# Kernel optimization log

Hardware: AMD Instinct MI355X
Metric: run time of the kernel (lower is better)

The kernel has to match this reference:

```python
import jax, jax.numpy as jnp
import numpy as np

N = 65536          # rays per batch
NC = 64            # coarse samples (config.num_samples_coarse)
NF = 128           # fine samples (config.num_samples_fine)
NEAR, FAR = 0.1, 1000.0


def setup_inputs() -> dict:
    key = jax.random.key(0)
    k = jax.random.split(key, 7)
    ray_origins = jax.random.normal(k[0], (N, 3), jnp.float32)
    ray_directions = jax.random.normal(k[1], (N, 3), jnp.float32)
    # stratified coarse t_vals == sample_points_along_rays(stratified=True)
    t = NEAR + (FAR - NEAR) * jnp.linspace(0.0, 1.0, NC, dtype=jnp.float32)
    t = jnp.broadcast_to(t, (N, NC))
    mids = 0.5 * (t[:, 1:] + t[:, :-1])
    upper = jnp.concatenate([mids, t[:, -1:]], axis=-1)
    lower = jnp.concatenate([t[:, :1], mids], axis=-1)
    t_rand = jax.random.uniform(k[2], (N, NC), jnp.float32)
    coarse_t_vals = lower + (upper - lower) * t_rand
    coarse_weights = jax.random.uniform(k[3], (N, NC), jnp.float32)
    u = jax.random.uniform(k[4], (N, NF), jnp.float32)
    colors = jax.random.uniform(k[5], (N, NC + NF, 3), jnp.float32)
    densities = jax.random.uniform(k[6], (N, NC + NF, 1), jnp.float32)
    return {"ray_origins": ray_origins, "ray_directions": ray_directions,
            "coarse_weights": coarse_weights, "coarse_t_vals": coarse_t_vals,
            "u": u, "colors": colors, "densities": densities}


def _hierarchical_sampling(ray_origins, ray_directions, coarse_weights, coarse_t_vals, u):
    # inverse-CDF importance resampling (GridNeRFRenderer.hierarchical_sampling)
    w = coarse_weights + 1e-5
    pdf = w / jnp.sum(w, axis=-1, keepdims=True)                 # [N, NC]
    cdf = jnp.cumsum(pdf, axis=-1)
    cdf = jnp.concatenate([jnp.zeros_like(cdf[..., :1]), cdf], axis=-1)  # [N, NC+1]
    # per-ray searchsorted (right)
    indices = jax.vmap(lambda c, uu: jnp.searchsorted(c, uu, side="right"))(cdf, u)  # [N, NF]
    nc = coarse_t_vals.shape[-1]
    below = jnp.clip(indices - 1, 0, nc - 1)
    above = jnp.clip(indices, 0, nc - 1)
    cdf_b = jnp.take_along_axis(cdf, below, axis=1)
    cdf_a = jnp.take_along_axis(cdf, above, axis=1)
    t_b = jnp.take_along_axis(coarse_t_vals, below, axis=1)
    t_a = jnp.take_along_axis(coarse_t_vals, above, axis=1)
    denom = cdf_a - cdf_b
    denom = jnp.where(denom < 1e-5, jnp.ones_like(denom), denom)
    tt = (u - cdf_b) / denom
    fine_t_vals = t_b + tt * (t_a - t_b)
    combined_t_vals = jnp.sort(jnp.concatenate([coarse_t_vals, fine_t_vals], axis=-1), axis=-1)  # [N, NC+NF]
    fine_points = ray_origins[:, None, :] + ray_directions[:, None, :] * combined_t_vals[..., None]
    return fine_points, combined_t_vals


def _volume_rendering(colors, densities, t_vals, ray_directions):
    dists = t_vals[..., 1:] - t_vals[..., :-1]
    dists = jnp.concatenate([dists, jnp.full_like(dists[..., :1], 1e10)], axis=-1)
    dists = dists * jnp.linalg.norm(ray_directions, axis=-1, keepdims=True)   # [N, S]
    alpha = 1.0 - jnp.exp(-densities[..., 0] * dists)                         # [N, S]
    # exclusive cumprod transmittance (== cumprod + roll + T[...,0]=1)
    trans = jnp.cumprod(1.0 - alpha + 1e-10, axis=-1)
    trans = jnp.concatenate([jnp.ones_like(trans[..., :1]), trans[..., :-1]], axis=-1)
    weights = alpha * trans
    rgb = jnp.sum(weights[..., None] * colors, axis=-2)   # [N, 3]
    depth = jnp.sum(weights * t_vals, axis=-1)            # [N]
    opacity = jnp.sum(weights, axis=-1)                   # [N]
    return rgb, depth, opacity, weights


def reference(ray_origins, ray_directions, coarse_weights, coarse_t_vals, u, colors, densities):
    fine_points, combined_t_vals = _hierarchical_sampling(
        ray_origins, ray_directions, coarse_weights, coarse_t_vals, u)
    rgb, depth, opacity, weights = _volume_rendering(
        colors, densities, combined_t_vals, ray_directions)
    return (rgb, depth, opacity, fine_points)
```

## Files before the change

kernel.cpp:

```cpp
#include <hip/hip_runtime.h>
#include <math.h>


#define NRAYS 65536
#define NCC   64
#define NFF   128
#define SS    192

__global__ __launch_bounds__(256)
void nerf_fused(const float* __restrict__ ro,  const float* __restrict__ rd,
                const float* __restrict__ cw,  const float* __restrict__ ct,
                const float* __restrict__ uu,  const float* __restrict__ col,
                const float* __restrict__ den, float* __restrict__ out)
{
    const int lane = threadIdx.x & 63;
    const int wv   = threadIdx.x >> 6;
    const int ray  = blockIdx.x * 4 + wv;

    __shared__ float s_cdf[4][65];
    __shared__ float s_ct [4][64];
    __shared__ float s_su [4][128];
    __shared__ float s_vals[4][256];

    float wt = cw[(size_t)ray * NCC + lane] + 1e-5f;
    float tc = ct[(size_t)ray * NCC + lane];
    float x = wt;
    #pragma unroll
    for (int off = 1; off < 64; off <<= 1) {
        float y = __shfl_up(x, off);
        if (lane >= off) x += y;
    }
    float total = __shfl(x, 63);
    float cv = x / total;
    #pragma unroll
    for (int off = 1; off < 64; off <<= 1) {
        float y = __shfl_up(cv, off);
        if (lane >= off) cv = fmaxf(cv, y);
    }
    s_cdf[wv][lane + 1] = cv;
    if (lane == 0) s_cdf[wv][0] = 0.0f;
    s_ct[wv][lane] = tc;

    float2 u2 = *(const float2*)(uu + (size_t)ray * NFF + 2 * lane);
    float v0 = u2.x, v1 = u2.y;
    #pragma unroll
    for (int k = 2; k <= 128; k <<= 1) {
        #pragma unroll
        for (int j = k >> 1; j >= 1; j >>= 1) {
            bool up = (((lane << 1) & k) == 0);
            if (j == 1) {
                float a = v0, b = v1;
                v0 = up ? fminf(a, b) : fmaxf(a, b);
                v1 = up ? fmaxf(a, b) : fminf(a, b);
            } else {
                int m = j >> 1;
                bool keepmin = (((lane & m) == 0) == up);
                float p0 = __shfl_xor(v0, m);
                float p1 = __shfl_xor(v1, m);
                v0 = keepmin ? fminf(v0, p0) : fmaxf(v0, p0);
                v1 = keepmin ? fminf(v1, p1) : fmaxf(v1, p1);
            }
        }
    }
    *(float2*)&s_su[wv][2 * lane] = make_float2(v0, v1);

    const float* cdfp = s_cdf[wv];
    const float* ctp  = s_ct[wv];
    float us[2] = {v0, v1};
    #pragma unroll
    for (int q = 0; q < 2; ++q) {
        float u = us[q];
        int pos = 0;
        #pragma unroll
        for (int st = 32; st >= 1; st >>= 1) {
            int np = pos + st;
            pos = (cdfp[np] <= u) ? np : pos;
        }
        int above = (pos + 1 < 63) ? (pos + 1) : 63;
        float cb = cdfp[pos], ca = cdfp[above];
        float tb = ctp[pos],  ta = ctp[above];
        float dnm = ca - cb;
        dnm = (dnm < 1e-5f) ? 1.0f : dnm;
        float tt = (u - cb) / dnm;
        float fval = tb + tt * (ta - tb);
        int rank = 2 * lane + q + pos + 1;
        s_vals[wv][rank] = fval;
    }

    const float* sup = s_su[wv];
    float key = cdfp[lane];
    int cnt = 0;
    #pragma unroll
    for (int st = 128; st >= 1; st >>= 1) {
        int np = cnt + st;
        bool ok = (np <= 128) && (sup[np - 1] < key);
        cnt = ok ? np : cnt;
    }
    s_vals[wv][lane + cnt] = tc;
    s_vals[wv][192 + lane] = 0.0f;

    float4 sv = *(const float4*)&s_vals[wv][4 * lane];
    float v[4] = {sv.x, sv.y, sv.z, sv.w};

    float dx = rd[(size_t)ray * 3 + 0], dy = rd[(size_t)ray * 3 + 1], dz = rd[(size_t)ray * 3 + 2];
    float ox = ro[(size_t)ray * 3 + 0], oy = ro[(size_t)ray * 3 + 1], oz = ro[(size_t)ray * 3 + 2];
    float nrm = sqrtf(dx * dx + dy * dy + dz * dz);

    const bool active = lane < 48;
    float tnext = __shfl_down(v[0], 1);
    float dd[4];
    dd[0] = v[1] - v[0];
    dd[1] = v[2] - v[1];
    dd[2] = v[3] - v[2];
    dd[3] = (lane == 47) ? 1e10f : (tnext - v[3]);

    float4 dn4 = make_float4(0.f, 0.f, 0.f, 0.f);
    if (active) dn4 = *(const float4*)(den + (size_t)ray * SS + 4 * lane);
    float dnv[4] = {dn4.x, dn4.y, dn4.z, dn4.w};

    float aa[4], ff[4];
    #pragma unroll
    for (int r = 0; r < 4; ++r) {
        float al = active ? (1.0f - expf(-dnv[r] * (dd[r] * nrm))) : 0.0f;
        aa[r] = al;
        ff[r] = active ? (1.0f - al + 1e-10f) : 1.0f;
    }

    if (active) {
        float* fp = out + (size_t)5 * NRAYS + (size_t)ray * (SS * 3) + 12 * lane;
        float4 p0 = make_float4(ox + dx * v[0], oy + dy * v[0], oz + dz * v[0], ox + dx * v[1]);
        float4 p1 = make_float4(oy + dy * v[1], oz + dz * v[1], ox + dx * v[2], oy + dy * v[2]);
        float4 p2 = make_float4(oz + dz * v[2], ox + dx * v[3], oy + dy * v[3], oz + dz * v[3]);
        *(float4*)(fp + 0) = p0;
        *(float4*)(fp + 4) = p1;
        *(float4*)(fp + 8) = p2;
    }

    float pr1 = ff[0], pr2 = ff[0] * ff[1], pr3 = pr2 * ff[2];
    float sx = pr3 * ff[3];
    #pragma unroll
    for (int off = 1; off < 64; off <<= 1) {
        float y = __shfl_up(sx, off);
        if (lane >= off) sx *= y;
    }
    float excl = __shfl_up(sx, 1);
    if (lane == 0) excl = 1.0f;
    float w0 = aa[0] * excl;
    float w1 = aa[1] * (excl * pr1);
    float w2 = aa[2] * (excl * pr2);
    float w3 = aa[3] * (excl * pr3);

    float4 c0 = make_float4(0.f,0.f,0.f,0.f), c1 = c0, c2 = c0;
    if (active) {
        const float* cp = col + (size_t)ray * (SS * 3) + 12 * lane;
        c0 = *(const float4*)(cp + 0);
        c1 = *(const float4*)(cp + 4);
        c2 = *(const float4*)(cp + 8);
    }
    float rr  = w0 * c0.x + w1 * c0.w + w2 * c1.z + w3 * c2.y;
    float gg  = w0 * c0.y + w1 * c1.x + w2 * c1.w + w3 * c2.z;
    float bb  = w0 * c0.z + w1 * c1.y + w2 * c2.x + w3 * c2.w;
    float dep = w0 * v[0] + w1 * v[1] + w2 * v[2] + w3 * v[3];
    float opa = w0 + w1 + w2 + w3;

    #pragma unroll
    for (int off = 32; off >= 1; off >>= 1) {
        rr  += __shfl_xor(rr,  off);
        gg  += __shfl_xor(gg,  off);
        bb  += __shfl_xor(bb,  off);
        dep += __shfl_xor(dep, off);
        opa += __shfl_xor(opa, off);
    }
    if (lane == 0) {
        out[(size_t)ray * 3 + 0] = rr;
        out[(size_t)ray * 3 + 1] = gg;
        out[(size_t)ray * 3 + 2] = bb;
        out[(size_t)3 * NRAYS + ray] = dep;
        out[(size_t)4 * NRAYS + ray] = opa;
    }
}

extern "C" void kernel_launch(void* const* d_in, const int* in_sizes, int n_in,
                              void* d_out, int out_size, void* d_ws, size_t ws_size,
                              hipStream_t stream) {
    const float* ro  = (const float*)d_in[0];
    const float* rd  = (const float*)d_in[1];
    const float* cw  = (const float*)d_in[2];
    const float* ct  = (const float*)d_in[3];
    const float* uu  = (const float*)d_in[4];
    const float* col = (const float*)d_in[5];
    const float* den = (const float*)d_in[6];
    float* out = (float*)d_out;
    (void)in_sizes; (void)n_in; (void)out_size; (void)d_ws; (void)ws_size;
    nerf_fused<<<NRAYS / 4, 256, 0, stream>>>(ro, rd, cw, ct, uu, col, den, out);
}
```

Measured before the change: 344.6 us.

## Use all 64 lanes with 3 samples each and prefetch global loads early

Remaps the rendering phase from 48 active lanes handling 4 samples each to all 64 lanes handling 3 samples each, using 12-byte struct loads and stores instead of float4. All global loads (u, ray origin and direction, densities, colors) are hoisted to the kernel start so their latency overlaps the CDF scan, bitonic sort and searchsorted work. It also switches expf to the fast __expf and computes 1-alpha directly from the exponential. The trade-offs are unaligned 12-byte accesses that may split into narrower memory instructions, higher register pressure from holding the early loads, and the reduced accuracy of __expf.

```diff
diff --git a/kernel.cpp b/kernel.cpp
--- a/kernel.cpp
+++ b/kernel.cpp
@@ -6,6 +6,8 @@
 #define NCC   64
 #define NFF   128
 #define SS    192
+
+struct f3 { float x, y, z; };
 
 __global__ __launch_bounds__(256)
 void nerf_fused(const float* __restrict__ ro,  const float* __restrict__ rd,
@@ -20,10 +22,19 @@
     __shared__ float s_cdf[4][65];
     __shared__ float s_ct [4][64];
     __shared__ float s_su [4][128];
-    __shared__ float s_vals[4][256];
+    __shared__ float s_vals[4][192];
 
     float wt = cw[(size_t)ray * NCC + lane] + 1e-5f;
     float tc = ct[(size_t)ray * NCC + lane];
+    float2 u2 = *(const float2*)(uu + (size_t)ray * NFF + 2 * lane);
+    float dx = rd[(size_t)ray * 3 + 0], dy = rd[(size_t)ray * 3 + 1], dz = rd[(size_t)ray * 3 + 2];
+    float ox = ro[(size_t)ray * 3 + 0], oy = ro[(size_t)ray * 3 + 1], oz = ro[(size_t)ray * 3 + 2];
+    f3 dn = *(const f3*)(den + (size_t)ray * SS + 3 * lane);
+    const float* cp = col + (size_t)ray * (SS * 3) + 9 * lane;
+    f3 c0 = *(const f3*)(cp + 0);
+    f3 c1 = *(const f3*)(cp + 3);
+    f3 c2 = *(const f3*)(cp + 6);
+
     float x = wt;
     #pragma unroll
     for (int off = 1; off < 64; off <<= 1) {
@@ -41,7 +52,6 @@
     if (lane == 0) s_cdf[wv][0] = 0.0f;
     s_ct[wv][lane] = tc;
 
-    float2 u2 = *(const float2*)(uu + (size_t)ray * NFF + 2 * lane);
     float v0 = u2.x, v1 = u2.y;
     #pragma unroll
     for (int k = 2; k <= 128; k <<= 1) {
@@ -97,47 +107,36 @@
         cnt = ok ? np : cnt;
     }
     s_vals[wv][lane + cnt] = tc;
-    s_vals[wv][192 + lane] = 0.0f;
 
-    float4 sv = *(const float4*)&s_vals[wv][4 * lane];
-    float v[4] = {sv.x, sv.y, sv.z, sv.w};
+    float v0s = s_vals[wv][3 * lane + 0];
+    float v1s = s_vals[wv][3 * lane + 1];
+    float v2s = s_vals[wv][3 * lane + 2];
 
-    float dx = rd[(size_t)ray * 3 + 0], dy = rd[(size_t)ray * 3 + 1], dz = rd[(size_t)ray * 3 + 2];
-    float ox = ro[(size_t)ray * 3 + 0], oy = ro[(size_t)ray * 3 + 1], oz = ro[(size_t)ray * 3 + 2];
     float nrm = sqrtf(dx * dx + dy * dy + dz * dz);
 
-    const bool active = lane < 48;
-    float tnext = __shfl_down(v[0], 1);
-    float dd[4];
-    dd[0] = v[1] - v[0];
-    dd[1] = v[2] - v[1];
-    dd[2] = v[3] - v[2];
-    dd[3] = (lane == 47) ? 1e10f : (tnext - v[3]);
+    float tnext = __shfl_down(v0s, 1);
+    float d0 = v1s - v0s;
+    float d1 = v2s - v1s;
+    float d2 = (lane == 63) ? 1e10f : (tnext - v2s);
 
-    float4 dn4 = make_float4(0.f, 0.f, 0.f, 0.f);
-    if (active) dn4 = *(const float4*)(den + (size_t)ray * SS + 4 * lane);
-    float dnv[4] = {dn4.x, dn4.y, dn4.z, dn4.w};
+    float e0 = __expf(-dn.x * (d0 * nrm));
+    float e1 = __expf(-dn.y * (d1 * nrm));
+    float e2 = __expf(-dn.z * (d2 * nrm));
+    float a0 = 1.0f - e0, a1 = 1.0f - e1, a2 = 1.0f - e2;
+    float f0 = e0 + 1e-10f, f1 = e1 + 1e-10f, f2 = e2 + 1e-10f;
 
-    float aa[4], ff[4];
-    #pragma unroll
-    for (int r = 0; r < 4; ++r) {
-        float al = active ? (1.0f - expf(-dnv[r] * (dd[r] * nrm))) : 0.0f;
-        aa[r] = al;
-        ff[r] = active ? (1.0f - al + 1e-10f) : 1.0f;
+    {
+        float* fp = out + (size_t)5 * NRAYS + (size_t)ray * (SS * 3) + 9 * lane;
+        f3 p0 = {ox + dx * v0s, oy + dy * v0s, oz + dz * v0s};
+        f3 p1 = {ox + dx * v1s, oy + dy * v1s, oz + dz * v1s};
+        f3 p2 = {ox + dx * v2s, oy + dy * v2s, oz + dz * v2s};
+        ((f3*)fp)[0] = p0;
+        ((f3*)fp)[1] = p1;
+        ((f3*)fp)[2] = p2;
     }
 
-    if (active) {
-        float* fp = out + (size_t)5 * NRAYS + (size_t)ray * (SS * 3) + 12 * lane;
-        float4 p0 = make_float4(ox + dx * v[0], oy + dy * v[0], oz + dz * v[0], ox + dx * v[1]);
-        float4 p1 = make_float4(oy + dy * v[1], oz + dz * v[1], ox + dx * v[2], oy + dy * v[2]);
-        float4 p2 = make_float4(oz + dz * v[2], ox + dx * v[3], oy + dy * v[3], oz + dz * v[3]);
-        *(float4*)(fp + 0) = p0;
-        *(float4*)(fp + 4) = p1;
-        *(float4*)(fp + 8) = p2;
-    }
-
-    float pr1 = ff[0], pr2 = ff[0] * ff[1], pr3 = pr2 * ff[2];
-    float sx = pr3 * ff[3];
+    float pr1 = f0, pr2 = f0 * f1;
+    float sx = pr2 * f2;
     #pragma unroll
     for (int off = 1; off < 64; off <<= 1) {
         float y = __shfl_up(sx, off);
@@ -145,23 +144,15 @@
     }
     float excl = __shfl_up(sx, 1);
     if (lane == 0) excl = 1.0f;
-    float w0 = aa[0] * excl;
-    float w1 = aa[1] * (excl * pr1);
-    float w2 = aa[2] * (excl * pr2);
-    float w3 = aa[3] * (excl * pr3);
+    float w0 = a0 * excl;
+    float w1 = a1 * (excl * pr1);
+    float w2 = a2 * (excl * pr2);
 
-    float4 c0 = make_float4(0.f,0.f,0.f,0.f), c1 = c0, c2 = c0;
-    if (active) {
-        const float* cp = col + (size_t)ray * (SS * 3) + 12 * lane;
-        c0 = *(const float4*)(cp + 0);
-        c1 = *(const float4*)(cp + 4);
-        c2 = *(const float4*)(cp + 8);
-    }
-    float rr  = w0 * c0.x + w1 * c0.w + w2 * c1.z + w3 * c2.y;
-    float gg  = w0 * c0.y + w1 * c1.x + w2 * c1.w + w3 * c2.z;
-    float bb  = w0 * c0.z + w1 * c1.y + w2 * c2.x + w3 * c2.w;
-    float dep = w0 * v[0] + w1 * v[1] + w2 * v[2] + w3 * v[3];
-    float opa = w0 + w1 + w2 + w3;
+    float rr  = w0 * c0.x + w1 * c1.x + w2 * c2.x;
+    float gg  = w0 * c0.y + w1 * c1.y + w2 * c2.y;
+    float bb  = w0 * c0.z + w1 * c1.z + w2 * c2.z;
+    float dep = w0 * v0s + w1 * v1s + w2 * v2s;
+    float opa = w0 + w1 + w2;
 
     #pragma unroll
     for (int off = 32; off >= 1; off >>= 1) {
```

New measurement: 345.1 us. About the same (+0.2%).
